# Kernel tuning notes

Hardware: AMD Instinct MI355X
Metric: run time of the kernel (lower is better)

Reference implementation:

```python
import jax, jax.numpy as jnp
import numpy as np
from jax import lax

B, C, H, W = 32, 128, 64, 64
K, KH, KW = 4, 3, 3
STRIDE = (1, 1)
PAD = [(1, 1), (1, 1)]


def setup_inputs() -> dict:
    key = jax.random.key(0)
    k1, k2, k3, k4 = jax.random.split(key, 4)
    x = jax.random.normal(k1, (B, C, H, W), dtype=jnp.float32)
    kernels = jax.random.normal(k2, (K, C, C, KH, KW), dtype=jnp.float32)
    fc_w = jax.random.normal(k3, (K, C), dtype=jnp.float32) * (1.0 / np.sqrt(C))
    fc_b = jax.random.normal(k4, (K,), dtype=jnp.float32) * 0.01
    return {"x": x, "kernels": kernels, "fc_w": fc_w, "fc_b": fc_b}


def reference(x, kernels, fc_w, fc_b):
    b, c, h, w = x.shape
    # DynamicRoutingLayer: GAP -> Linear -> sigmoid, then softmax over kernels
    pooled = x.mean(axis=(2, 3))                      # [B, C]
    coeffs = jax.nn.sigmoid(pooled @ fc_w.T + fc_b)   # [B, K]
    coeffs = jax.nn.softmax(coeffs, axis=1)
    # Per-sample mixed kernels: [B, C_out, C_in, kh, kw]
    dyn_k = jnp.einsum('bk,klmij->blmij', coeffs, kernels)
    # Batched per-sample conv via grouped conv: groups = batch
    xg = x.reshape(1, b * c, h, w)
    wg = dyn_k.reshape(b * c, c, KH, KW)
    out = lax.conv_general_dilated(
        xg, wg, window_strides=STRIDE, padding=PAD,
        dimension_numbers=('NCHW', 'OIHW', 'NCHW'),
        feature_group_count=b)
    return out.reshape(b, c, out.shape[2], out.shape[3])
```

## Files before the change

kernel.cpp:

```cpp
#include <hip/hip_runtime.h>
#include <math.h>

typedef __attribute__((ext_vector_type(8))) short s16x8;
typedef __attribute__((ext_vector_type(4))) float f32x4;
typedef __attribute__((ext_vector_type(4))) unsigned int u32x4;

#define CCH 128
#define BSZ 32

static __device__ inline unsigned short f2bf(float f) {
    unsigned u = __float_as_uint(f);
    unsigned r = (u + 0x7FFFu + ((u >> 16) & 1u)) >> 16;
    return (unsigned short)r;
}

__global__ __launch_bounds__(256) void pool_kernel(const float* __restrict__ x,
                                                   float* __restrict__ pooled) {
    int blk = blockIdx.x;
    const float4* x4 = (const float4*)(x + (size_t)blk * 4096);
    int t = threadIdx.x;
    float s = 0.f;
#pragma unroll
    for (int j = 0; j < 4; ++j) {
        float4 v = x4[j * 256 + t];
        s += v.x + v.y + v.z + v.w;
    }
#pragma unroll
    for (int off = 32; off; off >>= 1) s += __shfl_xor(s, off, 64);
    __shared__ float red[4];
    if ((t & 63) == 0) red[t >> 6] = s;
    __syncthreads();
    if (t == 0) {
        float tot = red[0] + red[1] + red[2] + red[3];
        pooled[blk] = tot * (1.0f / 4096.0f);
    }
}

__global__ __launch_bounds__(128) void coeff_kernel(const float* __restrict__ pooled,
                                                    const float* __restrict__ fc_w,
                                                    const float* __restrict__ fc_b,
                                                    float* __restrict__ coeffs) {
    int t = threadIdx.x;
    int b = t >> 2, k = t & 3;
    const float4* p4 = (const float4*)(pooled + b * CCH);
    const float4* w4 = (const float4*)(fc_w + k * CCH);
    float dot = fc_b[k];
#pragma unroll
    for (int j = 0; j < 32; ++j) {
        float4 a = p4[j], w = w4[j];
        dot += a.x * w.x + a.y * w.y + a.z * w.z + a.w * w.w;
    }
    float s = 1.0f / (1.0f + expf(-dot));
    float m = s;
    m = fmaxf(m, __shfl_xor(m, 1, 64));
    m = fmaxf(m, __shfl_xor(m, 2, 64));
    float e = expf(s - m);
    float sum = e;
    sum += __shfl_xor(sum, 1, 64);
    sum += __shfl_xor(sum, 2, 64);
    coeffs[t] = e / sum;
}

__global__ __launch_bounds__(256) void mix_kernel(const float* __restrict__ kernels,
                                                  const float* __restrict__ coeffs,
                                                  unsigned short* __restrict__ wmix) {
    extern __shared__ float klds[];
    int bid = blockIdx.x;
    int bq = bid & 15;
    int rest = bid >> 4;
    int cog = rest & 7, cc = rest >> 3;
    int t = threadIdx.x;

    const int KSTR = CCH * CCH * 9;
    for (int s = t; s < 4 * 16 * 288; s += 256) {
        int k = s / 4608;
        int rem = s - k * 4608;
        int co = rem / 288;
        int i = rem - co * 288;
        klds[k * 4624 + co * 289 + i] =
            kernels[(size_t)k * KSTR + ((size_t)(cog * 16 + co) * CCH + cc * 32) * 9 + i];
    }
    __syncthreads();

    int wr = cog >> 2, mt = cog & 3;
#pragma unroll
    for (int jb = 0; jb < 2; ++jb) {
        int b = bq + jb * 16;
        float cf0 = coeffs[b * 4 + 0];
        float cf1 = coeffs[b * 4 + 1];
        float cf2 = coeffs[b * 4 + 2];
        float cf3 = coeffs[b * 4 + 3];
        for (int s = t; s < 576; s += 256) {
            int lane = s & 63;
            int tj = s >> 6;
            int dy = tj / 3, dx = tj - dy * 3;
            int col = lane & 15;
            int ci8 = (lane >> 4) * 8;
            unsigned short vals[8];
#pragma unroll
            for (int e = 0; e < 8; ++e) {
                int idx = col * 289 + (ci8 + e) * 9 + dy * 3 + dx;
                float v = cf0 * klds[idx]
                        + cf1 * klds[4624 + idx]
                        + cf2 * klds[2 * 4624 + idx]
                        + cf3 * klds[3 * 4624 + idx];
                vals[e] = f2bf(v);
            }
            int p = cc * 3 + dy;
            size_t off = (size_t)b * 147456
                       + ((size_t)((p * 3 + dx) * 2 + wr) * 4 + mt) * 512 + (size_t)lane * 8;
            *(s16x8*)&wmix[off] = *(const s16x8*)vals;
        }
    }
}

__global__ __launch_bounds__(512, 4) void conv_kernel(const float* __restrict__ x,
                                                      const unsigned short* __restrict__ wmix,
                                                      float* __restrict__ out) {
    __shared__ unsigned short xs[6 * 66 * 40];

    int bid = blockIdx.x;
    int b = bid & 31, ytile = bid >> 5;
    int y0 = ytile * 4;
    int t = threadIdx.x;
    int l = t & 63, w = t >> 6;
    int wr = w >> 2, wc = w & 3;
    int l15 = l & 15, g = l >> 4;

    const unsigned short* wb = wmix + (size_t)b * 147456;

    if (t < 240) {
        int row = t / 40;
        int colsel = (t / 20) & 1;
        int cpart = t % 20;
        *(unsigned*)&xs[(row * 66 + colsel * 65) * 40 + cpart * 2] = 0u;
    }

    f32x4 acc[4][4] = {};

    for (int cc = 0; cc < 4; ++cc) {
        __syncthreads();
#pragma unroll
        for (int i = 0; i < 3; ++i) {
            int slot = w + i * 8;
            int row = slot >> 2, colhi = slot & 3;
            int gx = colhi * 16 + l15;
            int gy = y0 + row - 1;
            float v[8];
#pragma unroll
            for (int j = 0; j < 8; ++j) v[j] = 0.f;
            if ((unsigned)gy < 64u) {
                const float* xp = x + (((size_t)b * CCH + cc * 32 + g * 8) * 64 + gy) * 64 + gx;
#pragma unroll
                for (int j = 0; j < 8; ++j) v[j] = xp[(size_t)j * 4096];
            }
            unsigned pk[4];
#pragma unroll
            for (int j = 0; j < 4; ++j)
                pk[j] = (unsigned)f2bf(v[2 * j]) | ((unsigned)f2bf(v[2 * j + 1]) << 16);
            *(u32x4*)&xs[(size_t)(row * 66 + gx + 1) * 40 + g * 8] = *(const u32x4*)pk;
        }
        __syncthreads();
#pragma unroll
        for (int dy = 0; dy < 3; ++dy) {
            int p = cc * 3 + dy;
            int xrow = wc + dy;
#pragma unroll
            for (int dx = 0; dx < 3; ++dx) {
                const unsigned short* wt = wb + ((size_t)((p * 3 + dx) * 2 + wr) * 4) * 512
                                              + (size_t)l * 8;
                s16x8 a[4];
#pragma unroll
                for (int mt = 0; mt < 4; ++mt)
                    a[mt] = *(const s16x8*)(wt + mt * 512);
#pragma unroll
                for (int nt = 0; nt < 4; ++nt) {
                    s16x8 bf = *(const s16x8*)&xs[(size_t)(xrow * 66 + nt * 16 + l15 + dx) * 40 + g * 8];
#pragma unroll
                    for (int mt = 0; mt < 4; ++mt)
                        acc[mt][nt] = __builtin_amdgcn_mfma_f32_16x16x32_bf16(
                            a[mt], bf, acc[mt][nt], 0, 0, 0);
                }
            }
        }
    }

    int gy = y0 + wc;
#pragma unroll
    for (int mt = 0; mt < 4; ++mt)
#pragma unroll
        for (int nt = 0; nt < 4; ++nt) {
            int gxo = nt * 16 + l15;
#pragma unroll
            for (int j = 0; j < 4; ++j) {
                int co = wr * 64 + mt * 16 + g * 4 + j;
                out[(((size_t)b * CCH + co) * 64 + gy) * 64 + gxo] = acc[mt][nt][j];
            }
        }
}

extern "C" void kernel_launch(void* const* d_in, const int* in_sizes, int n_in,
                              void* d_out, int out_size, void* d_ws, size_t ws_size,
                              hipStream_t stream) {
    const float* x       = (const float*)d_in[0];
    const float* kernels = (const float*)d_in[1];
    const float* fc_w    = (const float*)d_in[2];
    const float* fc_b    = (const float*)d_in[3];
    float* out = (float*)d_out;

    float* pooled = (float*)d_ws;
    float* coeffs = pooled + BSZ * CCH;
    unsigned short* wmix = (unsigned short*)((char*)d_ws + 32768);

    hipFuncSetAttribute((const void*)mix_kernel,
                        hipFuncAttributeMaxDynamicSharedMemorySize, 73984);

    pool_kernel<<<BSZ * CCH, 256, 0, stream>>>(x, pooled);
    coeff_kernel<<<1, 128, 0, stream>>>(pooled, fc_w, fc_b, coeffs);
    mix_kernel<<<512, 256, 73984, stream>>>(kernels, coeffs, wmix);
    conv_kernel<<<512, 512, 0, stream>>>(x, wmix, out);
}
```

Measured before the change: 78.20 us.

## Halve conv row tile, prefetch next channel chunk and weights, use packed bf16 convert

The conv kernel now processes 2 output rows per block instead of 4, doubling the grid to 1024 blocks, and splits the N dimension across warps so each warp holds a 4x2 accumulator instead of 4x4. It register-prefetches the next 32-channel input chunk from global memory while the current chunk's MFMAs run, and it double-buffers the weight fragments for the next tap. The fp32-to-bf16 conversion now uses the hardware v_cvt_pk_bf16_f32 instruction. The intent is to improve occupancy and hide global-load latency, at the cost of more halo recomputation (4 rows loaded per 2 output rows) and more redundant weight reads across blocks.

```diff
diff --git a/kernel.cpp b/kernel.cpp
--- a/kernel.cpp
+++ b/kernel.cpp
@@ -12,6 +12,12 @@
     unsigned u = __float_as_uint(f);
     unsigned r = (u + 0x7FFFu + ((u >> 16) & 1u)) >> 16;
     return (unsigned short)r;
+}
+
+static __device__ inline unsigned cvtpk(float lo, float hi) {
+    unsigned r;
+    asm("v_cvt_pk_bf16_f32 %0, %1, %2" : "=v"(r) : "v"(lo), "v"(hi));
+    return r;
 }
 
 __global__ __launch_bounds__(256) void pool_kernel(const float* __restrict__ x,
@@ -117,71 +123,118 @@
 __global__ __launch_bounds__(512, 4) void conv_kernel(const float* __restrict__ x,
                                                       const unsigned short* __restrict__ wmix,
                                                       float* __restrict__ out) {
-    __shared__ unsigned short xs[6 * 66 * 40];
+    __shared__ unsigned short xs[4 * 66 * 40];
 
     int bid = blockIdx.x;
     int b = bid & 31, ytile = bid >> 5;
-    int y0 = ytile * 4;
+    int y0 = ytile * 2;
     int t = threadIdx.x;
     int l = t & 63, w = t >> 6;
-    int wr = w >> 2, wc = w & 3;
+    int wr = w >> 2;
+    int wc = (w >> 1) & 1;
+    int wn = w & 1;
     int l15 = l & 15, g = l >> 4;
 
     const unsigned short* wb = wmix + (size_t)b * 147456;
 
-    if (t < 240) {
+    if (t < 160) {
         int row = t / 40;
         int colsel = (t / 20) & 1;
         int cpart = t % 20;
         *(unsigned*)&xs[(row * 66 + colsel * 65) * 40 + cpart * 2] = 0u;
     }
 
-    f32x4 acc[4][4] = {};
+#pragma unroll
+    for (int i = 0; i < 2; ++i) {
+        int slot = w + i * 8;
+        int row = slot >> 2, colhi = slot & 3;
+        int gx = colhi * 16 + l15;
+        int gy = y0 + row - 1;
+        float v[8];
+#pragma unroll
+        for (int j = 0; j < 8; ++j) v[j] = 0.f;
+        if ((unsigned)gy < 64u) {
+            const float* xp = x + (((size_t)b * CCH + g * 8) * 64 + gy) * 64 + gx;
+#pragma unroll
+            for (int j = 0; j < 8; ++j) v[j] = xp[(size_t)j * 4096];
+        }
+        unsigned pw[4];
+#pragma unroll
+        for (int j = 0; j < 4; ++j) pw[j] = cvtpk(v[2 * j], v[2 * j + 1]);
+        u32x4 q; q[0] = pw[0]; q[1] = pw[1]; q[2] = pw[2]; q[3] = pw[3];
+        *(u32x4*)&xs[(size_t)(row * 66 + gx + 1) * 40 + g * 8] = q;
+    }
+    __syncthreads();
+
+    f32x4 acc[4][2] = {};
+    float xv[2][8];
+    unsigned pk[2][4];
 
     for (int cc = 0; cc < 4; ++cc) {
+        s16x8 a[4], n[4];
+        {
+            const unsigned short* wt = wb + ((size_t)((cc * 3) * 3) * 2 + wr) * 2048 + (size_t)l * 8;
+#pragma unroll
+            for (int mt = 0; mt < 4; ++mt) a[mt] = *(const s16x8*)(wt + mt * 512);
+        }
+        if (cc < 3) {
+#pragma unroll
+            for (int i = 0; i < 2; ++i) {
+                int slot = w + i * 8;
+                int row = slot >> 2, colhi = slot & 3;
+                int gx = colhi * 16 + l15;
+                int gy = y0 + row - 1;
+#pragma unroll
+                for (int j = 0; j < 8; ++j) xv[i][j] = 0.f;
+                if ((unsigned)gy < 64u) {
+                    const float* xp = x + (((size_t)b * CCH + (cc + 1) * 32 + g * 8) * 64 + gy) * 64 + gx;
+#pragma unroll
+                    for (int j = 0; j < 8; ++j) xv[i][j] = xp[(size_t)j * 4096];
+                }
+            }
+        }
+#pragma unroll
+        for (int tap = 0; tap < 9; ++tap) {
+            int dy = tap / 3, dx = tap - dy * 3;
+            if (tap < 8) {
+                int tap2 = tap + 1;
+                int dy2 = tap2 / 3, dx2 = tap2 - dy2 * 3;
+                const unsigned short* wt = wb + ((size_t)((cc * 3 + dy2) * 3 + dx2) * 2 + wr) * 2048
+                                              + (size_t)l * 8;
+#pragma unroll
+                for (int mt = 0; mt < 4; ++mt) n[mt] = *(const s16x8*)(wt + mt * 512);
+            }
+            int xrow = wc + dy;
+            s16x8 b0 = *(const s16x8*)&xs[(size_t)(xrow * 66 + wn * 32 + l15 + dx) * 40 + g * 8];
+            s16x8 b1 = *(const s16x8*)&xs[(size_t)(xrow * 66 + wn * 32 + 16 + l15 + dx) * 40 + g * 8];
+#pragma unroll
+            for (int mt = 0; mt < 4; ++mt) {
+                acc[mt][0] = __builtin_amdgcn_mfma_f32_16x16x32_bf16(a[mt], b0, acc[mt][0], 0, 0, 0);
+                acc[mt][1] = __builtin_amdgcn_mfma_f32_16x16x32_bf16(a[mt], b1, acc[mt][1], 0, 0, 0);
+            }
+            if (tap < 8) {
+#pragma unroll
+                for (int mt = 0; mt < 4; ++mt) a[mt] = n[mt];
+            }
+        }
+        if (cc < 3) {
+#pragma unroll
+            for (int i = 0; i < 2; ++i)
+#pragma unroll
+                for (int j = 0; j < 4; ++j)
+                    pk[i][j] = cvtpk(xv[i][2 * j], xv[i][2 * j + 1]);
+        }
         __syncthreads();
-#pragma unroll
-        for (int i = 0; i < 3; ++i) {
-            int slot = w + i * 8;
-            int row = slot >> 2, colhi = slot & 3;
-            int gx = colhi * 16 + l15;
-            int gy = y0 + row - 1;
-            float v[8];
-#pragma unroll
-            for (int j = 0; j < 8; ++j) v[j] = 0.f;
-            if ((unsigned)gy < 64u) {
-                const float* xp = x + (((size_t)b * CCH + cc * 32 + g * 8) * 64 + gy) * 64 + gx;
-#pragma unroll
-                for (int j = 0; j < 8; ++j) v[j] = xp[(size_t)j * 4096];
-            }
-            unsigned pk[4];
-#pragma unroll
-            for (int j = 0; j < 4; ++j)
-                pk[j] = (unsigned)f2bf(v[2 * j]) | ((unsigned)f2bf(v[2 * j + 1]) << 16);
-            *(u32x4*)&xs[(size_t)(row * 66 + gx + 1) * 40 + g * 8] = *(const u32x4*)pk;
-        }
-        __syncthreads();
-#pragma unroll
-        for (int dy = 0; dy < 3; ++dy) {
-            int p = cc * 3 + dy;
-            int xrow = wc + dy;
-#pragma unroll
-            for (int dx = 0; dx < 3; ++dx) {
-                const unsigned short* wt = wb + ((size_t)((p * 3 + dx) * 2 + wr) * 4) * 512
-                                              + (size_t)l * 8;
-                s16x8 a[4];
-#pragma unroll
-                for (int mt = 0; mt < 4; ++mt)
-                    a[mt] = *(const s16x8*)(wt + mt * 512);
-#pragma unroll
-                for (int nt = 0; nt < 4; ++nt) {
-                    s16x8 bf = *(const s16x8*)&xs[(size_t)(xrow * 66 + nt * 16 + l15 + dx) * 40 + g * 8];
-#pragma unroll
-                    for (int mt = 0; mt < 4; ++mt)
-                        acc[mt][nt] = __builtin_amdgcn_mfma_f32_16x16x32_bf16(
-                            a[mt], bf, acc[mt][nt], 0, 0, 0);
-                }
-            }
+        if (cc < 3) {
+#pragma unroll
+            for (int i = 0; i < 2; ++i) {
+                int slot = w + i * 8;
+                int row = slot >> 2, colhi = slot & 3;
+                int gx = colhi * 16 + l15;
+                u32x4 q; q[0] = pk[i][0]; q[1] = pk[i][1]; q[2] = pk[i][2]; q[3] = pk[i][3];
+                *(u32x4*)&xs[(size_t)(row * 66 + gx + 1) * 40 + g * 8] = q;
+            }
+            __syncthreads();
         }
     }
 
@@ -189,12 +242,12 @@
 #pragma unroll
     for (int mt = 0; mt < 4; ++mt)
 #pragma unroll
-        for (int nt = 0; nt < 4; ++nt) {
-            int gxo = nt * 16 + l15;
+        for (int ntl = 0; ntl < 2; ++ntl) {
+            int gxo = (wn * 2 + ntl) * 16 + l15;
 #pragma unroll
             for (int j = 0; j < 4; ++j) {
                 int co = wr * 64 + mt * 16 + g * 4 + j;
-                out[(((size_t)b * CCH + co) * 64 + gy) * 64 + gxo] = acc[mt][nt][j];
+                out[(((size_t)b * CCH + co) * 64 + gy) * 64 + gxo] = acc[mt][ntl][j];
             }
         }
 }
@@ -218,5 +271,5 @@
     pool_kernel<<<BSZ * CCH, 256, 0, stream>>>(x, pooled);
     coeff_kernel<<<1, 128, 0, stream>>>(pooled, fc_w, fc_b, coeffs);
     mix_kernel<<<512, 256, 73984, stream>>>(kernels, coeffs, wmix);
-    conv_kernel<<<512, 512, 0, stream>>>(x, wmix, out);
-}
+    conv_kernel<<<1024, 512, 0, stream>>>(x, wmix, out);
+}
```

After: 94.36 us. +20.7%, slower.

## Double-buffer conv input tile in LDS and prefetch next channel chunk

Applied to the files above, without the earlier changes.

The conv kernel now keeps two LDS buffers for the bf16 input tile. It issues the global loads for the next 32-channel chunk into registers before the MFMA loop on the current chunk, then converts and stores them into the other buffer afterwards, so each chunk needs one barrier instead of two. The float-to-bf16 packing also switches from software rounding to the hardware v_cvt_pk_bf16_f32 instruction. The cost is double the LDS per block and 24 extra live registers, which may reduce occupancy under the 512-thread, 4-blocks-per-CU launch bounds.

```diff
diff --git a/kernel.cpp b/kernel.cpp
--- a/kernel.cpp
+++ b/kernel.cpp
@@ -12,6 +12,12 @@
     unsigned u = __float_as_uint(f);
     unsigned r = (u + 0x7FFFu + ((u >> 16) & 1u)) >> 16;
     return (unsigned short)r;
+}
+
+static __device__ inline unsigned cvtpk(float lo, float hi) {
+    unsigned r;
+    asm("v_cvt_pk_bf16_f32 %0, %1, %2" : "=v"(r) : "v"(lo), "v"(hi));
+    return r;
 }
 
 __global__ __launch_bounds__(256) void pool_kernel(const float* __restrict__ x,
@@ -117,7 +123,7 @@
 __global__ __launch_bounds__(512, 4) void conv_kernel(const float* __restrict__ x,
                                                       const unsigned short* __restrict__ wmix,
                                                       float* __restrict__ out) {
-    __shared__ unsigned short xs[6 * 66 * 40];
+    __shared__ unsigned short xs[2][6 * 66 * 40];
 
     int bid = blockIdx.x;
     int b = bid & 31, ytile = bid >> 5;
@@ -129,38 +135,61 @@
 
     const unsigned short* wb = wmix + (size_t)b * 147456;
 
-    if (t < 240) {
-        int row = t / 40;
-        int colsel = (t / 20) & 1;
-        int cpart = t % 20;
-        *(unsigned*)&xs[(row * 66 + colsel * 65) * 40 + cpart * 2] = 0u;
-    }
+    if (t < 480) {
+        int buf = t / 240;
+        int r = t - buf * 240;
+        int row = r / 40;
+        int colsel = (r / 20) & 1;
+        int cpart = r % 20;
+        *(unsigned*)&xs[buf][(row * 66 + colsel * 65) * 40 + cpart * 2] = 0u;
+    }
+
+#pragma unroll
+    for (int i = 0; i < 3; ++i) {
+        int slot = w + i * 8;
+        int row = slot >> 2, colhi = slot & 3;
+        int gx = colhi * 16 + l15;
+        int gy = y0 + row - 1;
+        float v[8];
+#pragma unroll
+        for (int j = 0; j < 8; ++j) v[j] = 0.f;
+        if ((unsigned)gy < 64u) {
+            const float* xp = x + (((size_t)b * CCH + g * 8) * 64 + gy) * 64 + gx;
+#pragma unroll
+            for (int j = 0; j < 8; ++j) v[j] = xp[(size_t)j * 4096];
+        }
+        unsigned pw[4];
+#pragma unroll
+        for (int j = 0; j < 4; ++j) pw[j] = cvtpk(v[2 * j], v[2 * j + 1]);
+        u32x4 q; q[0] = pw[0]; q[1] = pw[1]; q[2] = pw[2]; q[3] = pw[3];
+        *(u32x4*)&xs[0][(size_t)(row * 66 + gx + 1) * 40 + g * 8] = q;
+    }
+    __syncthreads();
 
     f32x4 acc[4][4] = {};
+    float xv[3][8];
 
     for (int cc = 0; cc < 4; ++cc) {
-        __syncthreads();
-#pragma unroll
-        for (int i = 0; i < 3; ++i) {
-            int slot = w + i * 8;
-            int row = slot >> 2, colhi = slot & 3;
-            int gx = colhi * 16 + l15;
-            int gy = y0 + row - 1;
-            float v[8];
-#pragma unroll
-            for (int j = 0; j < 8; ++j) v[j] = 0.f;
-            if ((unsigned)gy < 64u) {
-                const float* xp = x + (((size_t)b * CCH + cc * 32 + g * 8) * 64 + gy) * 64 + gx;
-#pragma unroll
-                for (int j = 0; j < 8; ++j) v[j] = xp[(size_t)j * 4096];
-            }
-            unsigned pk[4];
-#pragma unroll
-            for (int j = 0; j < 4; ++j)
-                pk[j] = (unsigned)f2bf(v[2 * j]) | ((unsigned)f2bf(v[2 * j + 1]) << 16);
-            *(u32x4*)&xs[(size_t)(row * 66 + gx + 1) * 40 + g * 8] = *(const u32x4*)pk;
-        }
-        __syncthreads();
+        const unsigned short* xcur = xs[cc & 1];
+        unsigned short* xnxt = xs[(cc + 1) & 1];
+
+        if (cc < 3) {
+#pragma unroll
+            for (int i = 0; i < 3; ++i) {
+                int slot = w + i * 8;
+                int row = slot >> 2, colhi = slot & 3;
+                int gx = colhi * 16 + l15;
+                int gy = y0 + row - 1;
+#pragma unroll
+                for (int j = 0; j < 8; ++j) xv[i][j] = 0.f;
+                if ((unsigned)gy < 64u) {
+                    const float* xp = x + (((size_t)b * CCH + (cc + 1) * 32 + g * 8) * 64 + gy) * 64 + gx;
+#pragma unroll
+                    for (int j = 0; j < 8; ++j) xv[i][j] = xp[(size_t)j * 4096];
+                }
+            }
+        }
+
 #pragma unroll
         for (int dy = 0; dy < 3; ++dy) {
             int p = cc * 3 + dy;
@@ -175,7 +204,7 @@
                     a[mt] = *(const s16x8*)(wt + mt * 512);
 #pragma unroll
                 for (int nt = 0; nt < 4; ++nt) {
-                    s16x8 bf = *(const s16x8*)&xs[(size_t)(xrow * 66 + nt * 16 + l15 + dx) * 40 + g * 8];
+                    s16x8 bf = *(const s16x8*)&xcur[(size_t)(xrow * 66 + nt * 16 + l15 + dx) * 40 + g * 8];
 #pragma unroll
                     for (int mt = 0; mt < 4; ++mt)
                         acc[mt][nt] = __builtin_amdgcn_mfma_f32_16x16x32_bf16(
@@ -183,6 +212,21 @@
                 }
             }
         }
+
+        if (cc < 3) {
+#pragma unroll
+            for (int i = 0; i < 3; ++i) {
+                int slot = w + i * 8;
+                int row = slot >> 2, colhi = slot & 3;
+                int gx = colhi * 16 + l15;
+                unsigned pw[4];
+#pragma unroll
+                for (int j = 0; j < 4; ++j) pw[j] = cvtpk(xv[i][2 * j], xv[i][2 * j + 1]);
+                u32x4 q; q[0] = pw[0]; q[1] = pw[1]; q[2] = pw[2]; q[3] = pw[3];
+                *(u32x4*)&xnxt[(size_t)(row * 66 + gx + 1) * 40 + g * 8] = q;
+            }
+        }
+        __syncthreads();
     }
 
     int gy = y0 + wc;
```

After: 107.3 us. +37.2%, slower.

## Prepack x to channel-last bf16 and double-buffer conv input via global_load_lds

Applied to the files above, without the earlier changes.

A new prep kernel fuses global pooling with converting x into a channel-last bf16 workspace laid out with swizzled octets, producing partial sums per quarter that the coefficient kernel finishes. The conv kernel then streams input tiles straight into a double-buffered LDS using direct global-to-LDS loads, so the next channel chunk loads while MFMAs run on the current one. It also drops the per-block fp32-to-bf16 conversion and the redundant halo re-reads. The cost is an extra 32 MB workspace write plus read, and a fallback path is kept for when the workspace is too small.

```diff
diff --git a/kernel.cpp b/kernel.cpp
--- a/kernel.cpp
+++ b/kernel.cpp
@@ -14,42 +14,88 @@
     return (unsigned short)r;
 }
 
-__global__ __launch_bounds__(256) void pool_kernel(const float* __restrict__ x,
-                                                   float* __restrict__ pooled) {
-    int blk = blockIdx.x;
-    const float4* x4 = (const float4*)(x + (size_t)blk * 4096);
-    int t = threadIdx.x;
-    float s = 0.f;
+static __device__ inline unsigned cvtpk(float lo, float hi) {
+    unsigned r;
+    asm("v_cvt_pk_bf16_f32 %0, %1, %2" : "=v"(r) : "v"(lo), "v"(hi));
+    return r;
+}
+
+
+__global__ __launch_bounds__(256, 4) void prep_kernel(const float* __restrict__ x,
+                                                      unsigned short* __restrict__ xws,
+                                                      float* __restrict__ pooled2,
+                                                      unsigned short* __restrict__ zeros) {
+    int bid = blockIdx.x;
+    int t = threadIdx.x;
+    if (bid == 512) {
+        u32x4 zq = {0u, 0u, 0u, 0u};
+        *(u32x4*)&zeros[t * 8] = zq;
+        return;
+    }
+    int b = bid >> 4, cc = (bid >> 2) & 3, q = bid & 3;
+    const float* xb = x + ((size_t)b * CCH + cc * 32) * 4096;
+    unsigned short* xo = xws + (((size_t)b * 4 + cc) * 4096) * 32;
+
+    float sums[32];
+#pragma unroll
+    for (int c = 0; c < 32; ++c) sums[c] = 0.f;
+
 #pragma unroll
     for (int j = 0; j < 4; ++j) {
-        float4 v = x4[j * 256 + t];
-        s += v.x + v.y + v.z + v.w;
-    }
-#pragma unroll
-    for (int off = 32; off; off >>= 1) s += __shfl_xor(s, off, 64);
-    __shared__ float red[4];
-    if ((t & 63) == 0) red[t >> 6] = s;
+        int px = q * 1024 + j * 256 + t;
+        float v[32];
+#pragma unroll
+        for (int c = 0; c < 32; ++c) {
+            v[c] = xb[(size_t)c * 4096 + px];
+            sums[c] += v[c];
+        }
+        unsigned pw[16];
+#pragma unroll
+        for (int c2 = 0; c2 < 16; ++c2) pw[c2] = cvtpk(v[2 * c2], v[2 * c2 + 1]);
+        unsigned short* dp = xo + (size_t)px * 32;
+#pragma unroll
+        for (int o = 0; o < 4; ++o) {
+            u32x4 qv; qv[0] = pw[o*4+0]; qv[1] = pw[o*4+1]; qv[2] = pw[o*4+2]; qv[3] = pw[o*4+3];
+            *(u32x4*)&dp[o * 8] = qv;
+        }
+    }
+    __shared__ float red[4][32];
+    int l = t & 63, wv = t >> 6;
+#pragma unroll
+    for (int c = 0; c < 32; ++c) {
+        float s = sums[c];
+        s += __shfl_xor(s, 1, 64); s += __shfl_xor(s, 2, 64); s += __shfl_xor(s, 4, 64);
+        s += __shfl_xor(s, 8, 64); s += __shfl_xor(s, 16, 64); s += __shfl_xor(s, 32, 64);
+        if (l == 0) red[wv][c] = s;
+    }
     __syncthreads();
-    if (t == 0) {
-        float tot = red[0] + red[1] + red[2] + red[3];
-        pooled[blk] = tot * (1.0f / 4096.0f);
-    }
-}
-
-__global__ __launch_bounds__(128) void coeff_kernel(const float* __restrict__ pooled,
-                                                    const float* __restrict__ fc_w,
-                                                    const float* __restrict__ fc_b,
-                                                    float* __restrict__ coeffs) {
+    if (t < 32) {
+        float tot = red[0][t] + red[1][t] + red[2][t] + red[3][t];
+        pooled2[((size_t)b * 4 + q) * CCH + cc * 32 + t] = tot;
+    }
+}
+
+__global__ __launch_bounds__(128) void coeff2_kernel(const float* __restrict__ pooled2,
+                                                     const float* __restrict__ fc_w,
+                                                     const float* __restrict__ fc_b,
+                                                     float* __restrict__ coeffs) {
     int t = threadIdx.x;
     int b = t >> 2, k = t & 3;
-    const float4* p4 = (const float4*)(pooled + b * CCH);
+    const float4* p0 = (const float4*)(pooled2 + ((size_t)b * 4 + 0) * CCH);
+    const float4* p1 = (const float4*)(pooled2 + ((size_t)b * 4 + 1) * CCH);
+    const float4* p2 = (const float4*)(pooled2 + ((size_t)b * 4 + 2) * CCH);
+    const float4* p3 = (const float4*)(pooled2 + ((size_t)b * 4 + 3) * CCH);
     const float4* w4 = (const float4*)(fc_w + k * CCH);
-    float dot = fc_b[k];
+    float acc = 0.f;
 #pragma unroll
     for (int j = 0; j < 32; ++j) {
-        float4 a = p4[j], w = w4[j];
-        dot += a.x * w.x + a.y * w.y + a.z * w.z + a.w * w.w;
-    }
+        float4 a0 = p0[j], a1 = p1[j], a2 = p2[j], a3 = p3[j], w = w4[j];
+        acc += (a0.x + a1.x + a2.x + a3.x) * w.x;
+        acc += (a0.y + a1.y + a2.y + a3.y) * w.y;
+        acc += (a0.z + a1.z + a2.z + a3.z) * w.z;
+        acc += (a0.w + a1.w + a2.w + a3.w) * w.w;
+    }
+    float dot = fc_b[k] + acc * (1.0f / 4096.0f);
     float s = 1.0f / (1.0f + expf(-dot));
     float m = s;
     m = fmaxf(m, __shfl_xor(m, 1, 64));
@@ -114,10 +160,165 @@
     }
 }
 
-__global__ __launch_bounds__(512, 4) void conv_kernel(const float* __restrict__ x,
+__global__ __launch_bounds__(512, 4) void conv_kernel(const unsigned short* __restrict__ xws,
                                                       const unsigned short* __restrict__ wmix,
+                                                      const unsigned short* __restrict__ zeros,
                                                       float* __restrict__ out) {
-    __shared__ unsigned short xs[6 * 66 * 40];
+    __shared__ unsigned short xs[2][13824];
+
+    int bid = blockIdx.x;
+    int b = bid & 31, ytile = bid >> 5;
+    int y0 = ytile * 4;
+    int t = threadIdx.x;
+    int l = t & 63, w = t >> 6;
+    int wr = w >> 2, wc = w & 3;
+    int l15 = l & 15, g = l >> 4;
+
+    const unsigned short* wb = wmix + (size_t)b * 147456;
+
+    const unsigned short* psrc[4];
+    int pvalid = 0;
+#pragma unroll
+    for (int k = 0; k < 4; ++k) {
+        int s = w + k * 8;
+        int slot = s * 64 + l;
+        int oct_s = slot & 3;
+        int cp = (slot >> 2) % 72;
+        int row = (slot >> 2) / 72;
+        int gy = y0 + row - 1;
+        int gx = cp - 2;
+        int octL = oct_s ^ ((cp >> 1) & 3);
+        if (s < 27 && (unsigned)gy < 64u && (unsigned)gx < 64u) {
+            psrc[k] = xws + (((size_t)b * 4 * 64 + gy) * 64 + gx) * 32 + octL * 8;
+            pvalid |= (1 << k);
+        } else {
+            psrc[k] = zeros + l * 8;
+        }
+    }
+
+#pragma unroll
+    for (int k = 0; k < 4; ++k) {
+        int s = w + k * 8;
+        if (s < 27) {
+            __builtin_amdgcn_global_load_lds(
+                (const __attribute__((address_space(1))) void*)psrc[k],
+                (__attribute__((address_space(3))) void*)(&xs[0][0] + s * 512 + l * 8), 16, 0, 0);
+        }
+    }
+    __syncthreads();
+
+    f32x4 acc[4][4] = {};
+
+    for (int cc = 0; cc < 4; ++cc) {
+        const unsigned short* xcur = &xs[cc & 1][0];
+        if (cc < 3) {
+            unsigned short* xnxt = &xs[(cc + 1) & 1][0];
+#pragma unroll
+            for (int k = 0; k < 4; ++k) {
+                int s = w + k * 8;
+                if (s < 27) {
+                    const unsigned short* sp = psrc[k]
+                        + (((pvalid >> k) & 1) ? (size_t)(cc + 1) * 131072 : (size_t)0);
+                    __builtin_amdgcn_global_load_lds(
+                        (const __attribute__((address_space(1))) void*)sp,
+                        (__attribute__((address_space(3))) void*)(xnxt + s * 512 + l * 8), 16, 0, 0);
+                }
+            }
+        }
+#pragma unroll
+        for (int dy = 0; dy < 3; ++dy) {
+            int p = cc * 3 + dy;
+            int xrow = wc + dy;
+#pragma unroll
+            for (int dx = 0; dx < 3; ++dx) {
+                const unsigned short* wt = wb + ((size_t)((p * 3 + dx) * 2 + wr) * 4) * 512
+                                              + (size_t)l * 8;
+                s16x8 a[4];
+#pragma unroll
+                for (int mt = 0; mt < 4; ++mt)
+                    a[mt] = *(const s16x8*)(wt + mt * 512);
+#pragma unroll
+                for (int nt = 0; nt < 4; ++nt) {
+                    int cp = nt * 16 + l15 + dx + 1;
+                    s16x8 bf = *(const s16x8*)&xcur[(size_t)(xrow * 72 + cp) * 32
+                                                    + (g ^ ((cp >> 1) & 3)) * 8];
+#pragma unroll
+                    for (int mt = 0; mt < 4; ++mt)
+                        acc[mt][nt] = __builtin_amdgcn_mfma_f32_16x16x32_bf16(
+                            a[mt], bf, acc[mt][nt], 0, 0, 0);
+                }
+            }
+        }
+        __syncthreads();
+    }
+
+    int gy = y0 + wc;
+#pragma unroll
+    for (int mt = 0; mt < 4; ++mt)
+#pragma unroll
+        for (int nt = 0; nt < 4; ++nt) {
+            int gxo = nt * 16 + l15;
+#pragma unroll
+            for (int j = 0; j < 4; ++j) {
+                int co = wr * 64 + mt * 16 + g * 4 + j;
+                out[(((size_t)b * CCH + co) * 64 + gy) * 64 + gxo] = acc[mt][nt][j];
+            }
+        }
+}
+
+
+__global__ __launch_bounds__(256) void pool_kernel(const float* __restrict__ x,
+                                                   float* __restrict__ pooled) {
+    int blk = blockIdx.x;
+    const float4* x4 = (const float4*)(x + (size_t)blk * 4096);
+    int t = threadIdx.x;
+    float s = 0.f;
+#pragma unroll
+    for (int j = 0; j < 4; ++j) {
+        float4 v = x4[j * 256 + t];
+        s += v.x + v.y + v.z + v.w;
+    }
+#pragma unroll
+    for (int off = 32; off; off >>= 1) s += __shfl_xor(s, off, 64);
+    __shared__ float red[4];
+    if ((t & 63) == 0) red[t >> 6] = s;
+    __syncthreads();
+    if (t == 0) {
+        float tot = red[0] + red[1] + red[2] + red[3];
+        pooled[blk] = tot * (1.0f / 4096.0f);
+    }
+}
+
+__global__ __launch_bounds__(128) void coeff_kernel(const float* __restrict__ pooled,
+                                                    const float* __restrict__ fc_w,
+                                                    const float* __restrict__ fc_b,
+                                                    float* __restrict__ coeffs) {
+    int t = threadIdx.x;
+    int b = t >> 2, k = t & 3;
+    const float4* p4 = (const float4*)(pooled + b * CCH);
+    const float4* w4 = (const float4*)(fc_w + k * CCH);
+    float dot = fc_b[k];
+#pragma unroll
+    for (int j = 0; j < 32; ++j) {
+        float4 a = p4[j], w = w4[j];
+        dot += a.x * w.x + a.y * w.y + a.z * w.z + a.w * w.w;
+    }
+    float s = 1.0f / (1.0f + expf(-dot));
+    float m = s;
+    m = fmaxf(m, __shfl_xor(m, 1, 64));
+    m = fmaxf(m, __shfl_xor(m, 2, 64));
+    float e = expf(s - m);
+    float sum = e;
+    sum += __shfl_xor(sum, 1, 64);
+    sum += __shfl_xor(sum, 2, 64);
+    coeffs[t] = e / sum;
+}
+
+typedef __attribute__((ext_vector_type(4))) unsigned int u32x4b;
+__global__ __launch_bounds__(512, 4) void conv_fb_kernel(const float* __restrict__ x,
+                                                         const unsigned short* __restrict__ wmix,
+                                                         float* __restrict__ out) {
+    __shared__ unsigned short xsb[6 * 66 * 40];
 
     int bid = blockIdx.x;
     int b = bid & 31, ytile = bid >> 5;
@@ -133,7 +334,7 @@
         int row = t / 40;
         int colsel = (t / 20) & 1;
         int cpart = t % 20;
-        *(unsigned*)&xs[(row * 66 + colsel * 65) * 40 + cpart * 2] = 0u;
+        *(unsigned*)&xsb[(row * 66 + colsel * 65) * 40 + cpart * 2] = 0u;
     }
 
     f32x4 acc[4][4] = {};
@@ -158,7 +359,8 @@
 #pragma unroll
             for (int j = 0; j < 4; ++j)
                 pk[j] = (unsigned)f2bf(v[2 * j]) | ((unsigned)f2bf(v[2 * j + 1]) << 16);
-            *(u32x4*)&xs[(size_t)(row * 66 + gx + 1) * 40 + g * 8] = *(const u32x4*)pk;
+            u32x4b qv; qv[0] = pk[0]; qv[1] = pk[1]; qv[2] = pk[2]; qv[3] = pk[3];
+            *(u32x4b*)&xsb[(size_t)(row * 66 + gx + 1) * 40 + g * 8] = qv;
         }
         __syncthreads();
 #pragma unroll
@@ -175,7 +377,7 @@
                     a[mt] = *(const s16x8*)(wt + mt * 512);
 #pragma unroll
                 for (int nt = 0; nt < 4; ++nt) {
-                    s16x8 bf = *(const s16x8*)&xs[(size_t)(xrow * 66 + nt * 16 + l15 + dx) * 40 + g * 8];
+                    s16x8 bf = *(const s16x8*)&xsb[(size_t)(xrow * 66 + nt * 16 + l15 + dx) * 40 + g * 8];
 #pragma unroll
                     for (int mt = 0; mt < 4; ++mt)
                         acc[mt][nt] = __builtin_amdgcn_mfma_f32_16x16x32_bf16(
@@ -208,15 +410,29 @@
     const float* fc_b    = (const float*)d_in[3];
     float* out = (float*)d_out;
 
-    float* pooled = (float*)d_ws;
-    float* coeffs = pooled + BSZ * CCH;
-    unsigned short* wmix = (unsigned short*)((char*)d_ws + 32768);
-
     hipFuncSetAttribute((const void*)mix_kernel,
                         hipFuncAttributeMaxDynamicSharedMemorySize, 73984);
 
-    pool_kernel<<<BSZ * CCH, 256, 0, stream>>>(x, pooled);
-    coeff_kernel<<<1, 128, 0, stream>>>(pooled, fc_w, fc_b, coeffs);
-    mix_kernel<<<512, 256, 73984, stream>>>(kernels, coeffs, wmix);
-    conv_kernel<<<512, 512, 0, stream>>>(x, wmix, out);
-}
+    const size_t NEED = 16777216ull + 33554432ull;
+    if (ws_size >= NEED) {
+        float* pooled2        = (float*)d_ws;
+        float* coeffs         = (float*)((char*)d_ws + 65536);
+        unsigned short* zeros = (unsigned short*)((char*)d_ws + 66560);
+        unsigned short* wmix  = (unsigned short*)((char*)d_ws + 73728);
+        unsigned short* xws   = (unsigned short*)((char*)d_ws + 16777216);
+
+        prep_kernel<<<513, 256, 0, stream>>>(x, xws, pooled2, zeros);
+        coeff2_kernel<<<1, 128, 0, stream>>>(pooled2, fc_w, fc_b, coeffs);
+        mix_kernel<<<512, 256, 73984, stream>>>(kernels, coeffs, wmix);
+        conv_kernel<<<512, 512, 0, stream>>>(xws, wmix, zeros, out);
+    } else {
+        float* pooled = (float*)d_ws;
+        float* coeffs = pooled + BSZ * CCH;
+        unsigned short* wmix = (unsigned short*)((char*)d_ws + 32768);
+
+        pool_kernel<<<BSZ * CCH, 256, 0, stream>>>(x, pooled);
+        coeff_kernel<<<1, 128, 0, stream>>>(pooled, fc_w, fc_b, coeffs);
+        mix_kernel<<<512, 256, 73984, stream>>>(kernels, coeffs, wmix);
+        conv_fb_kernel<<<512, 512, 0, stream>>>(x, wmix, out);
+    }
+}
```

After: 120.4 us. +54.0%, slower.
